# Kernel tuning notes

Measured on AMD Instinct MI355X. Metric: run time of the kernel, lower is better.

Reference implementation:

```python
import jax, jax.numpy as jnp
import numpy as np

K = 20  # kNN neighbors
HEADS = 4
DIM_HEAD = 32


def setup_inputs() -> dict:
    key = jax.random.key(0)
    ks = jax.random.split(key, 20)
    B, N = 8, 2048
    s = 0.05
    inp = {
        "x": jax.random.normal(ks[0], (B, N, 3), dtype=jnp.float32),
        "batch": jnp.zeros((B, N), dtype=jnp.int32),
        # EdgeConv1: Linear(2*3, 64) -> ReLU -> Linear(64, 64)
        "ec1_w1": jax.random.normal(ks[1], (6, 64), jnp.float32) * s,
        "ec1_b1": jnp.zeros((64,), jnp.float32),
        "ec1_w2": jax.random.normal(ks[2], (64, 64), jnp.float32) * s,
        "ec1_b2": jnp.zeros((64,), jnp.float32),
        # EdgeConv2: Linear(2*64, 64) -> ReLU -> Linear(64, 128)
        "ec2_w1": jax.random.normal(ks[3], (128, 64), jnp.float32) * s,
        "ec2_b1": jnp.zeros((64,), jnp.float32),
        "ec2_w2": jax.random.normal(ks[4], (64, 128), jnp.float32) * s,
        "ec2_b2": jnp.zeros((128,), jnp.float32),
        # SelfAttention: to_qkv Linear(128, 384, bias=False); fc_out Linear(128,128)
        "qkv_w": jax.random.normal(ks[5], (128, 384), jnp.float32) * s,
        "out_w": jax.random.normal(ks[6], (128, 128), jnp.float32) * s,
        "out_b": jnp.zeros((128,), jnp.float32),
        # refine MLP: 384 -> 128 -> 64 -> num_classes(20)
        "r1_w": jax.random.normal(ks[7], (384, 128), jnp.float32) * s,
        "r1_b": jnp.zeros((128,), jnp.float32),
        "r2_w": jax.random.normal(ks[8], (128, 64), jnp.float32) * s,
        "r2_b": jnp.zeros((64,), jnp.float32),
        "r3_w": jax.random.normal(ks[9], (64, 20), jnp.float32) * s,
        "r3_b": jnp.zeros((20,), jnp.float32),
    }
    return inp


def _edge_conv(x, w1, b1, w2, b2):
    # x: [B, N, C]. Dynamic kNN in feature space, edge feat [x_i, x_j - x_i],
    # MLP, max over neighbors.
    sq = jnp.sum(x * x, axis=-1)                       # [B, N]
    d = sq[:, :, None] + sq[:, None, :] - 2.0 * jnp.einsum("bnc,bmc->bnm", x, x)
    _, idx = jax.lax.top_k(-d, K)                      # [B, N, K]
    nbr = jax.vmap(lambda xb, ib: xb[ib])(x, idx)      # [B, N, K, C]
    xi = jnp.broadcast_to(x[:, :, None, :], nbr.shape)
    e = jnp.concatenate([xi, nbr - xi], axis=-1)       # [B, N, K, 2C]
    h = jax.nn.relu(e @ w1 + b1) @ w2 + b2             # [B, N, K, out]
    return jnp.max(h, axis=2)                          # [B, N, out]


def _attention(x, qkv_w, out_w, out_b):
    B, N, C = x.shape
    qkv = x @ qkv_w                                    # [B, N, 3C]
    q, k, v = jnp.split(qkv, 3, axis=-1)
    def heads(t):
        return t.reshape(B, N, HEADS, DIM_HEAD).transpose(0, 2, 1, 3)  # [B,H,N,Dh]
    q, k, v = heads(q), heads(k), heads(v)
    scale = DIM_HEAD ** -0.5
    attn = jax.nn.softmax(jnp.einsum("bhnd,bhmd->bhnm", q, k) * scale, axis=-1)
    out = jnp.einsum("bhnm,bhmd->bhnd", attn, v)
    out = out.transpose(0, 2, 1, 3).reshape(B, N, C)
    return out @ out_w + out_b


def reference(x, batch, ec1_w1, ec1_b1, ec1_w2, ec1_b2,
              ec2_w1, ec2_b1, ec2_w2, ec2_b2,
              qkv_w, out_w, out_b,
              r1_w, r1_b, r2_w, r2_b, r3_w, r3_b):
    local = _edge_conv(x, ec1_w1, ec1_b1, ec1_w2, ec1_b2)        # [B,N,64]
    local = _edge_conv(local, ec2_w1, ec2_b1, ec2_w2, ec2_b2)    # [B,N,128]
    glob = jnp.max(local, axis=1, keepdims=True)                 # [B,1,128]
    glob = jnp.broadcast_to(glob, local.shape)                   # [B,N,128]
    att = _attention(local, qkv_w, out_w, out_b)                 # [B,N,128]
    comb = jnp.concatenate([local, glob, att], axis=-1)          # [B,N,384]
    h = jax.nn.relu(comb @ r1_w + r1_b)
    h = jax.nn.relu(h @ r2_w + r2_b)
    logits = h @ r3_w + r3_b
    return jax.nn.log_softmax(logits, axis=-1)
```

## Files before the change

kernel.cpp:

```cpp
#include <hip/hip_runtime.h>
#include <hip/hip_bf16.h>

#define BB 8
#define NN 2048
#define KK 20
#define BBNN (BB * NN)

typedef __hip_bfloat16 bf16;
typedef unsigned short u16;
typedef __attribute__((ext_vector_type(8))) short short8;
typedef __attribute__((ext_vector_type(4))) float f32x4;

__device__ __forceinline__ float b2f(bf16 v) { return __bfloat162float(v); }

template<int C>
__global__ __launch_bounds__(256) void sqT_kernel(const float* __restrict__ xin,
                                                  float* __restrict__ sq,
                                                  float* __restrict__ xT) {
    int t = blockIdx.x * 256 + threadIdx.x;
    if (t >= BBNN) return;
    const float* p = xin + (size_t)t * C;
    float s = 0.f;
    for (int c = 0; c < C; ++c) {
        float v = p[c];
        s += v * v;
        xT[(size_t)c * BBNN + t] = v;
    }
    sq[t] = s;
}

template<int C>
__global__ __launch_bounds__(512, 4) void knn1_kernel(
        const float* __restrict__ xrows,
        const float* __restrict__ xT,
        const float* __restrict__ sq,
        u16* __restrict__ idx_out) {
    __shared__ __align__(16) float xs[C][2048];
    const int blk = blockIdx.x;
    const int b = blk >> 8;
    const int tile = blk & 255;
    const int w = threadIdx.x >> 6;
    const int s = threadIdx.x & 63;
    const int tid = threadIdx.x;
    const int iA = tile * 8 + w;
    const int bn0 = b * NN;

    float dA[32];
    #pragma unroll
    for (int r = 0; r < 32; ++r) dA[r] = 0.f;

    for (int u = tid; u < C * 512; u += 512) {
        int row = u / 512, c4 = u % 512;
        *(float4*)&xs[row][c4 * 4] =
            *(const float4*)(xT + (size_t)row * BBNN + bn0 + c4 * 4);
    }
    __syncthreads();

    const int qbase = __builtin_amdgcn_readfirstlane((bn0 + iA) * C);
    float xq[C];
    #pragma unroll
    for (int cc = 0; cc < C; ++cc) xq[cc] = xrows[qbase + cc];

    #pragma unroll
    for (int t = 0; t < 8; ++t) {
        float a0 = 0.f, a1 = 0.f, a2 = 0.f, a3 = 0.f;
        #pragma unroll
        for (int cc = 0; cc < C; ++cc) {
            float4 xv = *(const float4*)&xs[cc][t * 256 + s * 4];
            float q = xq[cc];
            a0 += q * xv.x; a1 += q * xv.y; a2 += q * xv.z; a3 += q * xv.w;
        }
        dA[t * 4 + 0] += a0; dA[t * 4 + 1] += a1;
        dA[t * 4 + 2] += a2; dA[t * 4 + 3] += a3;
    }
    const float sqi = sq[bn0 + iA];
    #pragma unroll
    for (int r = 0; r < 32; ++r) {
        int j = ((r >> 2) << 8) + (s << 2) + (r & 3);
        dA[r] = (sqi + sq[bn0 + j]) - 2.f * dA[r];
    }

    unsigned rm = 0u;
    float m1 = INFINITY, m2 = INFINITY;
    int j1 = 0x7fffffff, j2 = 0x7fffffff;
    #pragma unroll
    for (int r = 0; r < 32; ++r) {
        int j = ((r >> 2) << 8) + (s << 2) + (r & 3);
        float d = dA[r];
        bool l1 = d < m1, l2 = d < m2;
        m2 = l1 ? m1 : (l2 ? d : m2);
        j2 = l1 ? j1 : (l2 ? j : j2);
        m1 = l1 ? d : m1;  j1 = l1 ? j : j1;
    }
    for (int k = 0; k < KK; ++k) {
        if (__any(j1 < 0)) {
            if (j1 < 0) {
                m1 = INFINITY; m2 = INFINITY; j1 = 0x7fffffff; j2 = 0x7fffffff;
                #pragma unroll
                for (int r = 0; r < 32; ++r) {
                    int j = ((r >> 2) << 8) + (s << 2) + (r & 3);
                    float d = (rm & (1u << r)) ? INFINITY : dA[r];
                    bool l1 = d < m1, l2 = d < m2;
                    m2 = l1 ? m1 : (l2 ? d : m2);
                    j2 = l1 ? j1 : (l2 ? j : j2);
                    m1 = l1 ? d : m1;  j1 = l1 ? j : j1;
                }
            }
        }
        float rd = m1; int rj = j1;
        #pragma unroll
        for (int m = 1; m < 64; m <<= 1) {
            float od = __shfl_xor(rd, m); int oj = __shfl_xor(rj, m);
            if (od < rd || (od == rd && oj < rj)) { rd = od; rj = oj; }
        }
        if (s == 0) idx_out[(size_t)(bn0 + iA) * KK + k] = (u16)rj;
        if (k + 1 < KK) {
            if (s == ((rj >> 2) & 63)) {
                int rr = ((rj >> 8) << 2) + (rj & 3);
                rm |= (1u << rr);
                m1 = m2; j1 = j2; m2 = INFINITY; j2 = -1;
            }
        }
    }
}

template<int C, int CH>
__global__ __launch_bounds__(512, 4) void knn_fast_kernel(
        const float* __restrict__ xrows,
        const float* __restrict__ xT,
        const float* __restrict__ sq,
        u16* __restrict__ idx_out) {
    __shared__ __align__(16) float xs[CH][2048];
    const int blk = blockIdx.x;
    const int b = blk >> 7;
    const int tile = blk & 127;
    const int w = threadIdx.x >> 6;
    const int s = threadIdx.x & 63;
    const int iA = tile * 16 + w * 2;
    const int bn0 = b * NN;
    constexpr int NCH = C / CH;

    float dA[32], dB[32];
    #pragma unroll
    for (int r = 0; r < 32; ++r) { dA[r] = 0.f; dB[r] = 0.f; }

    const int qbase = __builtin_amdgcn_readfirstlane((bn0 + iA) * C);

    for (int ch = 0; ch < NCH; ++ch) {
        __syncthreads();
        for (int u = threadIdx.x; u < CH * 512; u += 512) {
            int row = u >> 9, c4 = u & 511;
            *(float4*)&xs[row][c4 * 4] =
                *(const float4*)(xT + (size_t)(ch * CH + row) * BBNN + bn0 + c4 * 4);
        }
        __syncthreads();
        float xqA[CH], xqB[CH];
        #pragma unroll
        for (int cc = 0; cc < CH; ++cc) {
            xqA[cc] = xrows[qbase + ch * CH + cc];
            xqB[cc] = xrows[qbase + C + ch * CH + cc];
        }
        #pragma unroll
        for (int t = 0; t < 8; ++t) {
            float aA0 = 0.f, aA1 = 0.f, aA2 = 0.f, aA3 = 0.f;
            float aB0 = 0.f, aB1 = 0.f, aB2 = 0.f, aB3 = 0.f;
            #pragma unroll
            for (int cc = 0; cc < CH; ++cc) {
                float4 xv = *(const float4*)&xs[cc][t * 256 + s * 4];
                float qA = xqA[cc], qB = xqB[cc];
                aA0 += qA * xv.x; aA1 += qA * xv.y; aA2 += qA * xv.z; aA3 += qA * xv.w;
                aB0 += qB * xv.x; aB1 += qB * xv.y; aB2 += qB * xv.z; aB3 += qB * xv.w;
            }
            dA[t * 4 + 0] += aA0; dA[t * 4 + 1] += aA1;
            dA[t * 4 + 2] += aA2; dA[t * 4 + 3] += aA3;
            dB[t * 4 + 0] += aB0; dB[t * 4 + 1] += aB1;
            dB[t * 4 + 2] += aB2; dB[t * 4 + 3] += aB3;
        }
    }
    const float sqiA = sq[bn0 + iA];
    const float sqiB = sq[bn0 + iA + 1];
    #pragma unroll
    for (int r = 0; r < 32; ++r) {
        int j = ((r >> 2) << 8) + (s << 2) + (r & 3);
        float sqj = sq[bn0 + j];
        dA[r] = (sqiA + sqj) - 2.f * dA[r];
        dB[r] = (sqiB + sqj) - 2.f * dB[r];
    }

    unsigned rmA = 0u, rmB = 0u;
    float m1A = INFINITY, m2A = INFINITY, m1B = INFINITY, m2B = INFINITY;
    int j1A = 0x7fffffff, j2A = 0x7fffffff, j1B = 0x7fffffff, j2B = 0x7fffffff;
    #pragma unroll
    for (int r = 0; r < 32; ++r) {
        int j = ((r >> 2) << 8) + (s << 2) + (r & 3);
        float d = dA[r];
        bool l1 = d < m1A, l2 = d < m2A;
        m2A = l1 ? m1A : (l2 ? d : m2A);
        j2A = l1 ? j1A : (l2 ? j : j2A);
        m1A = l1 ? d : m1A;  j1A = l1 ? j : j1A;
        d = dB[r];
        l1 = d < m1B; l2 = d < m2B;
        m2B = l1 ? m1B : (l2 ? d : m2B);
        j2B = l1 ? j1B : (l2 ? j : j2B);
        m1B = l1 ? d : m1B;  j1B = l1 ? j : j1B;
    }

    for (int k = 0; k < KK; ++k) {
        if (__any(j1A < 0)) {
            if (j1A < 0) {
                m1A = INFINITY; m2A = INFINITY; j1A = 0x7fffffff; j2A = 0x7fffffff;
                #pragma unroll
                for (int r = 0; r < 32; ++r) {
                    int j = ((r >> 2) << 8) + (s << 2) + (r & 3);
                    float d = (rmA & (1u << r)) ? INFINITY : dA[r];
                    bool l1 = d < m1A, l2 = d < m2A;
                    m2A = l1 ? m1A : (l2 ? d : m2A);
                    j2A = l1 ? j1A : (l2 ? j : j2A);
                    m1A = l1 ? d : m1A;  j1A = l1 ? j : j1A;
                }
            }
        }
        if (__any(j1B < 0)) {
            if (j1B < 0) {
                m1B = INFINITY; m2B = INFINITY; j1B = 0x7fffffff; j2B = 0x7fffffff;
                #pragma unroll
                for (int r = 0; r < 32; ++r) {
                    int j = ((r >> 2) << 8) + (s << 2) + (r & 3);
                    float d = (rmB & (1u << r)) ? INFINITY : dB[r];
                    bool l1 = d < m1B, l2 = d < m2B;
                    m2B = l1 ? m1B : (l2 ? d : m2B);
                    j2B = l1 ? j1B : (l2 ? j : j2B);
                    m1B = l1 ? d : m1B;  j1B = l1 ? j : j1B;
                }
            }
        }
        float rdA = m1A, rdB = m1B; int rjA = j1A, rjB = j1B;
        #pragma unroll
        for (int m = 1; m < 64; m <<= 1) {
            float odA = __shfl_xor(rdA, m); int ojA = __shfl_xor(rjA, m);
            float odB = __shfl_xor(rdB, m); int ojB = __shfl_xor(rjB, m);
            if (odA < rdA || (odA == rdA && ojA < rjA)) { rdA = odA; rjA = ojA; }
            if (odB < rdB || (odB == rdB && ojB < rjB)) { rdB = odB; rjB = ojB; }
        }
        if (s == 0) {
            idx_out[(size_t)(bn0 + iA) * KK + k]     = (u16)rjA;
            idx_out[(size_t)(bn0 + iA + 1) * KK + k] = (u16)rjB;
        }
        if (k + 1 < KK) {
            if (s == ((rjA >> 2) & 63)) {
                int rr = ((rjA >> 8) << 2) + (rjA & 3);
                rmA |= (1u << rr);
                m1A = m2A; j1A = j2A; m2A = INFINITY; j2A = -1;
            }
            if (s == ((rjB >> 2) & 63)) {
                int rr = ((rjB >> 8) << 2) + (rjB & 3);
                rmB |= (1u << rr);
                m1B = m2B; j1B = j2B; m2B = INFINITY; j2B = -1;
            }
        }
    }
}

template<int CIN>
__global__ __launch_bounds__(256) void gemmG_kernel(const float* __restrict__ xin,
                                                    const float* __restrict__ w1,
                                                    float* __restrict__ G) {
    __shared__ __align__(16) float xr[16][CIN];
    const int bn0 = blockIdx.x * 16;
    const int tid = threadIdx.x;
    for (int p = tid; p < 16 * CIN; p += 256)
        xr[p / CIN][p % CIN] = xin[(size_t)bn0 * CIN + p];
    const int h = tid & 63, rgrp = tid >> 6;
    float wcol[CIN];
    #pragma unroll
    for (int c = 0; c < CIN; ++c) wcol[c] = w1[(CIN + c) * 64 + h];
    __syncthreads();
    #pragma unroll
    for (int rq = 0; rq < 4; ++rq) {
        const int rr = rgrp + rq * 4;
        float a = 0.f;
        if constexpr (CIN % 4 == 0) {
            #pragma unroll
            for (int c4 = 0; c4 < CIN / 4; ++c4) {
                float4 hv = *(const float4*)&xr[rr][c4 * 4];
                a += hv.x * wcol[c4 * 4 + 0];
                a += hv.y * wcol[c4 * 4 + 1];
                a += hv.z * wcol[c4 * 4 + 2];
                a += hv.w * wcol[c4 * 4 + 3];
            }
        } else {
            #pragma unroll
            for (int c = 0; c < CIN; ++c) a += xr[rr][c] * wcol[c];
        }
        G[(size_t)(bn0 + rr) * 64 + h] = a;
    }
}

template<int CIN, int COUT, bool BF16OUT>
__global__ __launch_bounds__(256) void edgeconv3_kernel(
        const float* __restrict__ xin, const u16* __restrict__ knn,
        const float* __restrict__ w1, const float* __restrict__ b1,
        const float* __restrict__ w2, const float* __restrict__ b2,
        const float* __restrict__ G, void* __restrict__ out) {
    constexpr int NS = 4;
    constexpr int KPS = KK / NS;
    const int bn0 = blockIdx.x * 4;
    const int b = bn0 >> 11;
    const int tid = threadIdx.x;
    __shared__ __align__(16) float xr[4][CIN];
    __shared__ __align__(16) float h1s[4][KK][64];
    __shared__ float pms[4][NS][COUT];
    __shared__ int js[4][KK];

    for (int p = tid; p < 4 * CIN; p += 256)
        xr[p / CIN][p % CIN] = xin[(size_t)bn0 * CIN + p];
    if (tid < 4 * KK) {
        int j = knn[(size_t)(bn0 + tid / KK) * KK + (tid % KK)];
        js[tid / KK][tid % KK] = (j < NN) ? j : 0;
    }
    __syncthreads();

    {
        const int pp = tid >> 6, h = tid & 63;
        float w1col[CIN];
        #pragma unroll
        for (int c = 0; c < CIN; ++c) w1col[c] = w1[c * 64 + h];
        float u = b1[h];
        if constexpr (CIN % 4 == 0) {
            #pragma unroll
            for (int c4 = 0; c4 < CIN / 4; ++c4) {
                float4 hv = *(const float4*)&xr[pp][c4 * 4];
                u += hv.x * w1col[c4 * 4 + 0];
                u += hv.y * w1col[c4 * 4 + 1];
                u += hv.z * w1col[c4 * 4 + 2];
                u += hv.w * w1col[c4 * 4 + 3];
            }
        } else {
            #pragma unroll
            for (int c = 0; c < CIN; ++c) u += xr[pp][c] * w1col[c];
        }
        u -= G[(size_t)(bn0 + pp) * 64 + h];
        const float* Gb = G + (size_t)b * NN * 64 + h;
        for (int k = 0; k < KK; ++k) {
            float gj = Gb[(size_t)js[pp][k] * 64];
            h1s[pp][k][h] = fmaxf(u + gj, 0.f);
        }
    }
    __syncthreads();

    if constexpr (COUT == 128) {
        const int o = tid & 63, ks = tid >> 6;
        float wcolA[64], wcolB[64];
        #pragma unroll
        for (int c = 0; c < 64; ++c) {
            wcolA[c] = w2[c * COUT + o];
            wcolB[c] = w2[c * COUT + o + 64];
        }
        #pragma unroll
        for (int pp = 0; pp < 4; ++pp) {
            float mxA = -INFINITY, mxB = -INFINITY;
            for (int k = ks * KPS; k < (ks + 1) * KPS; ++k) {
                float accA = 0.f, accB = 0.f;
                #pragma unroll
                for (int c4 = 0; c4 < 16; ++c4) {
                    float4 hv = *(const float4*)&h1s[pp][k][c4 * 4];
                    accA += hv.x * wcolA[c4 * 4 + 0];
                    accA += hv.y * wcolA[c4 * 4 + 1];
                    accA += hv.z * wcolA[c4 * 4 + 2];
                    accA += hv.w * wcolA[c4 * 4 + 3];
                    accB += hv.x * wcolB[c4 * 4 + 0];
                    accB += hv.y * wcolB[c4 * 4 + 1];
                    accB += hv.z * wcolB[c4 * 4 + 2];
                    accB += hv.w * wcolB[c4 * 4 + 3];
                }
                mxA = fmaxf(mxA, accA);
                mxB = fmaxf(mxB, accB);
            }
            pms[pp][ks][o] = mxA;
            pms[pp][ks][o + 64] = mxB;
        }
    } else {
        const int o = tid % COUT, ks = tid / COUT;
        float wcol[64];
        #pragma unroll
        for (int c = 0; c < 64; ++c) wcol[c] = w2[c * COUT + o];
        #pragma unroll
        for (int pp = 0; pp < 4; ++pp) {
            float mx = -INFINITY;
            for (int k = ks * KPS; k < (ks + 1) * KPS; ++k) {
                float acc = 0.f;
                #pragma unroll
                for (int c4 = 0; c4 < 16; ++c4) {
                    float4 hv = *(const float4*)&h1s[pp][k][c4 * 4];
                    acc += hv.x * wcol[c4 * 4 + 0];
                    acc += hv.y * wcol[c4 * 4 + 1];
                    acc += hv.z * wcol[c4 * 4 + 2];
                    acc += hv.w * wcol[c4 * 4 + 3];
                }
                mx = fmaxf(mx, acc);
            }
            pms[pp][ks][o] = mx;
        }
    }
    __syncthreads();
    for (int idx = tid; idx < 4 * COUT; idx += 256) {
        int pp = idx / COUT, oo = idx % COUT;
        float mx = pms[pp][0][oo];
        #pragma unroll
        for (int s2 = 1; s2 < NS; ++s2) mx = fmaxf(mx, pms[pp][s2][oo]);
        mx += b2[oo];
        if (BF16OUT) ((bf16*)out)[(size_t)(bn0 + pp) * COUT + oo] = __float2bfloat16(mx);
        else         ((float*)out)[(size_t)(bn0 + pp) * COUT + oo] = mx;
    }
}

__global__ __launch_bounds__(128) void gmax1_kernel(const bf16* __restrict__ f2,
                                                    float* __restrict__ pmax) {
    const int b = blockIdx.x >> 4, ch = blockIdx.x & 15, c = threadIdx.x;
    float m = -INFINITY;
    const bf16* base = f2 + ((size_t)(b * NN + ch * 128)) * 128 + c;
    for (int n = 0; n < 128; ++n) m = fmaxf(m, b2f(base[(size_t)n * 128]));
    pmax[blockIdx.x * 128 + c] = m;
}

__global__ __launch_bounds__(128) void gmax2_kernel(const float* __restrict__ pmax,
                                                    float* __restrict__ glob) {
    const int b = blockIdx.x, c = threadIdx.x;
    float m = -INFINITY;
    for (int ch = 0; ch < 16; ++ch) m = fmaxf(m, pmax[(b * 16 + ch) * 128 + c]);
    glob[b * 128 + c] = m;
}

__global__ __launch_bounds__(256) void kvt_kernel(const bf16* __restrict__ f2,
                                                  const float* __restrict__ qkv_w,
                                                  bf16* __restrict__ kk,
                                                  bf16* __restrict__ vt) {
    const int blk = blockIdx.x;
    const int h = blk >> 10;
    const int rg = blk & 1023;
    const int bn0 = rg * 16;
    const int b = bn0 >> 11, n0 = bn0 & 2047;
    const int tid = threadIdx.x;
    __shared__ __align__(16) float f2s[16][128];
    __shared__ float vbuf[16][32];

    for (int p = tid; p < 16 * 128; p += 256) {
        int rr = p >> 7, c = p & 127;
        f2s[rr][c] = b2f(f2[(size_t)(bn0 + rr) * 128 + c]);
    }
    const int col = tid & 63, rgrp = tid >> 6;
    const int kv = col >> 5, d = col & 31;
    float wcol[128];
    #pragma unroll
    for (int c = 0; c < 128; ++c)
        wcol[c] = qkv_w[c * 384 + 128 + kv * 128 + h * 32 + d];
    __syncthreads();

    #pragma unroll
    for (int rq = 0; rq < 4; ++rq) {
        const int rr = rgrp + rq * 4;
        float acc = 0.f;
        #pragma unroll
        for (int c4 = 0; c4 < 32; ++c4) {
            float4 hv = *(const float4*)&f2s[rr][c4 * 4];
            acc += hv.x * wcol[c4 * 4 + 0];
            acc += hv.y * wcol[c4 * 4 + 1];
            acc += hv.z * wcol[c4 * 4 + 2];
            acc += hv.w * wcol[c4 * 4 + 3];
        }
        if (kv == 0)
            kk[((size_t)(b * 4 + h) * 2048 + n0 + rr) * 32 + d] = __float2bfloat16(acc);
        else
            vbuf[rr][d] = acc;
    }
    __syncthreads();
    if (tid < 128) {
        int dd = tid >> 2, r2 = tid & 3;
        #pragma unroll
        for (int rq = 0; rq < 4; ++rq) {
            int r = r2 + rq * 4;
            vt[((size_t)(b * 4 + h) * 32 + dd) * 2048 + n0 + r] = __float2bfloat16(vbuf[r][dd]);
        }
    }
}

__global__ __launch_bounds__(256) void attn_mfma_kernel(
        const bf16* __restrict__ f2, const float* __restrict__ qkv_w,
        const bf16* __restrict__ kk, const bf16* __restrict__ vt,
        bf16* __restrict__ atth) {
    const int blk = blockIdx.x;
    const int tile = blk & 31;
    const int h = (blk >> 5) & 3;
    const int b = blk >> 7;
    const int tid = threadIdx.x;
    const int w = tid >> 6;
    const int lane = tid & 63;
    const int lq = lane & 15;
    const int quad = lane >> 4;
    const float scale = 0.17677669529663687f;

    __shared__ __align__(16) bf16 WqT[32][128];
    __shared__ __align__(16) bf16 pbuf[4][2][16][32];

    for (int p = tid; p < 4096; p += 256) {
        int c = p >> 5, d = p & 31;
        WqT[d][c] = __float2bfloat16(qkv_w[c * 384 + h * 32 + d]);
    }
    __syncthreads();

    const int q0 = tile * 64 + w * 16;
    const bf16* fbase = f2 + ((size_t)(b * NN + q0 + lq)) * 128;
    f32x4 qc0 = {0.f, 0.f, 0.f, 0.f}, qc1 = {0.f, 0.f, 0.f, 0.f};
    #pragma unroll
    for (int kc = 0; kc < 4; ++kc) {
        short8 af = *(const short8*)(fbase + kc * 32 + quad * 8);
        short8 b0 = *(const short8*)(&WqT[lq][kc * 32 + quad * 8]);
        short8 b1 = *(const short8*)(&WqT[16 + lq][kc * 32 + quad * 8]);
        qc0 = __builtin_amdgcn_mfma_f32_16x16x32_bf16(af, b0, qc0, 0, 0, 0);
        qc1 = __builtin_amdgcn_mfma_f32_16x16x32_bf16(af, b1, qc1, 0, 0, 0);
    }
    {
        bf16* pw = &pbuf[w][0][0][0];
        #pragma unroll
        for (int r = 0; r < 4; ++r) {
            int qq = quad * 4 + r;
            pw[qq * 32 + lq]      = __float2bfloat16(qc0[r] * scale);
            pw[qq * 32 + 16 + lq] = __float2bfloat16(qc1[r] * scale);
        }
    }
    const short8 qfrag = *(const short8*)(&pbuf[w][0][lq][quad * 8]);

    const bf16* kb = kk + (size_t)(b * 4 + h) * 2048 * 32;
    const bf16* vb = vt + (size_t)(b * 4 + h) * 32 * 2048;
    f32x4 o0 = {0.f, 0.f, 0.f, 0.f}, o1 = {0.f, 0.f, 0.f, 0.f};
    f32x4 lsum = {0.f, 0.f, 0.f, 0.f};
    const short8 ones = {(short)0x3F80, (short)0x3F80, (short)0x3F80, (short)0x3F80,
                         (short)0x3F80, (short)0x3F80, (short)0x3F80, (short)0x3F80};

    for (int ch = 0; ch < 64; ++ch) {
        const int j0 = ch * 32;
        short8 kf0 = *(const short8*)(kb + (size_t)(j0 + lq) * 32 + quad * 8);
        short8 kf1 = *(const short8*)(kb + (size_t)(j0 + 16 + lq) * 32 + quad * 8);
        f32x4 z = {0.f, 0.f, 0.f, 0.f};
        f32x4 s0 = __builtin_amdgcn_mfma_f32_16x16x32_bf16(qfrag, kf0, z, 0, 0, 0);
        f32x4 s1 = __builtin_amdgcn_mfma_f32_16x16x32_bf16(qfrag, kf1, z, 0, 0, 0);
        bf16* pw = &pbuf[w][ch & 1][0][0];
        #pragma unroll
        for (int r = 0; r < 4; ++r) {
            int qq = quad * 4 + r;
            pw[qq * 32 + lq]      = __float2bfloat16(__expf(s0[r]));
            pw[qq * 32 + 16 + lq] = __float2bfloat16(__expf(s1[r]));
        }
        short8 pf = *(const short8*)(pw + lq * 32 + quad * 8);
        short8 vf0 = *(const short8*)(vb + (size_t)lq * 2048 + j0 + quad * 8);
        short8 vf1 = *(const short8*)(vb + (size_t)(16 + lq) * 2048 + j0 + quad * 8);
        o0   = __builtin_amdgcn_mfma_f32_16x16x32_bf16(pf, vf0, o0, 0, 0, 0);
        o1   = __builtin_amdgcn_mfma_f32_16x16x32_bf16(pf, vf1, o1, 0, 0, 0);
        lsum = __builtin_amdgcn_mfma_f32_16x16x32_bf16(pf, ones, lsum, 0, 0, 0);
    }

    #pragma unroll
    for (int r = 0; r < 4; ++r) {
        int row = q0 + quad * 4 + r;
        float inv = 1.f / lsum[r];
        bf16* orow = atth + ((size_t)(b * NN + row)) * 128 + h * 32;
        orow[lq]      = __float2bfloat16(o0[r] * inv);
        orow[16 + lq] = __float2bfloat16(o1[r] * inv);
    }
}

__global__ __launch_bounds__(256) void final_kernel(
        const bf16* __restrict__ f2, const float* __restrict__ glob,
        const bf16* __restrict__ atth,
        const float* __restrict__ out_w, const float* __restrict__ out_b,
        const float* __restrict__ r1_w, const float* __restrict__ r1_b,
        const float* __restrict__ r2_w, const float* __restrict__ r2_b,
        const float* __restrict__ r3_w, const float* __restrict__ r3_b,
        float* __restrict__ out) {
    const int bn0 = blockIdx.x * 8;
    const int b = bn0 >> 11;
    const int tid = threadIdx.x;
    __shared__ float attin[8][128], comb[8][384], h1[8][128], h2[8][64];
    __shared__ float logits[8][20], lse[8];

    for (int p = tid; p < 8 * 128; p += 256) {
        int rr = p >> 7, c = p & 127;
        attin[rr][c]      = b2f(atth[(size_t)(bn0 + rr) * 128 + c]);
        comb[rr][c]       = b2f(f2[(size_t)(bn0 + rr) * 128 + c]);
        comb[rr][128 + c] = glob[b * 128 + c];
    }
    __syncthreads();
    {
        const int col = tid & 127, r0 = (tid >> 7) * 4;
        float a0 = 0.f, a1 = 0.f, a2 = 0.f, a3 = 0.f;
        for (int c = 0; c < 128; ++c) {
            float wv = out_w[c * 128 + col];
            a0 += attin[r0 + 0][c] * wv; a1 += attin[r0 + 1][c] * wv;
            a2 += attin[r0 + 2][c] * wv; a3 += attin[r0 + 3][c] * wv;
        }
        float bb = out_b[col];
        comb[r0 + 0][256 + col] = a0 + bb; comb[r0 + 1][256 + col] = a1 + bb;
        comb[r0 + 2][256 + col] = a2 + bb; comb[r0 + 3][256 + col] = a3 + bb;
    }
    __syncthreads();
    {
        const int col = tid & 127, r0 = (tid >> 7) * 4;
        float a0 = 0.f, a1 = 0.f, a2 = 0.f, a3 = 0.f;
        for (int c = 0; c < 384; ++c) {
            float wv = r1_w[c * 128 + col];
            a0 += comb[r0 + 0][c] * wv; a1 += comb[r0 + 1][c] * wv;
            a2 += comb[r0 + 2][c] * wv; a3 += comb[r0 + 3][c] * wv;
        }
        float bb = r1_b[col];
        h1[r0 + 0][col] = fmaxf(a0 + bb, 0.f); h1[r0 + 1][col] = fmaxf(a1 + bb, 0.f);
        h1[r0 + 2][col] = fmaxf(a2 + bb, 0.f); h1[r0 + 3][col] = fmaxf(a3 + bb, 0.f);
    }
    __syncthreads();
    {
        const int col = tid & 63, r0 = (tid >> 6) * 2;
        float a0 = 0.f, a1 = 0.f;
        for (int c = 0; c < 128; ++c) {
            float wv = r2_w[c * 64 + col];
            a0 += h1[r0 + 0][c] * wv; a1 += h1[r0 + 1][c] * wv;
        }
        float bb = r2_b[col];
        h2[r0 + 0][col] = fmaxf(a0 + bb, 0.f); h2[r0 + 1][col] = fmaxf(a1 + bb, 0.f);
    }
    __syncthreads();
    if (tid < 160) {
        const int cls = tid % 20, rr = tid / 20;
        float a0 = 0.f;
        for (int c = 0; c < 64; ++c) a0 += h2[rr][c] * r3_w[c * 20 + cls];
        logits[rr][cls] = a0 + r3_b[cls];
    }
    __syncthreads();
    if (tid < 8) {
        float m = -INFINITY;
        for (int u = 0; u < 20; ++u) m = fmaxf(m, logits[tid][u]);
        float s = 0.f;
        for (int u = 0; u < 20; ++u) s += expf(logits[tid][u] - m);
        lse[tid] = m + logf(s);
    }
    __syncthreads();
    if (tid < 160) {
        int rr = tid / 20, cls = tid % 20;
        out[(size_t)(bn0 + rr) * 20 + cls] = logits[rr][cls] - lse[rr];
    }
}

extern "C" void kernel_launch(void* const* d_in, const int* in_sizes, int n_in,
                              void* d_out, int out_size, void* d_ws, size_t ws_size,
                              hipStream_t stream) {
    const float* x      = (const float*)d_in[0];
    const float* ec1_w1 = (const float*)d_in[2];
    const float* ec1_b1 = (const float*)d_in[3];
    const float* ec1_w2 = (const float*)d_in[4];
    const float* ec1_b2 = (const float*)d_in[5];
    const float* ec2_w1 = (const float*)d_in[6];
    const float* ec2_b1 = (const float*)d_in[7];
    const float* ec2_w2 = (const float*)d_in[8];
    const float* ec2_b2 = (const float*)d_in[9];
    const float* qkv_w  = (const float*)d_in[10];
    const float* out_w  = (const float*)d_in[11];
    const float* out_b  = (const float*)d_in[12];
    const float* r1_w   = (const float*)d_in[13];
    const float* r1_b   = (const float*)d_in[14];
    const float* r2_w   = (const float*)d_in[15];
    const float* r2_b   = (const float*)d_in[16];
    const float* r3_w   = (const float*)d_in[17];
    const float* r3_b   = (const float*)d_in[18];
    float* out = (float*)d_out;

    const size_t MB = 1024 * 1024;
    const size_t NEED_A = 16 * MB + 65536 + 4096;
    if (ws_size < NEED_A) return;

    char* base = (char*)d_ws;
    bf16*  f2   = (bf16*)(base);
    float* f1T  = (float*)(base);
    float* sqb  = (float*)(base + 4 * MB);
    float* f1   = (float*)(base + 4 * MB + 65536);
    u16*   knn  = (u16*)(base + 8 * MB + 65536);
    float* xT3  = (float*)(base + 8 * MB + 65536 + 655360);
    float* G    = (float*)(base + 12 * MB);
    bf16*  kkA  = (bf16*)(base + 4 * MB);
    bf16*  vtA  = (bf16*)(base + 8 * MB);
    bf16*  atth = (bf16*)(base + 12 * MB);
    float* pmax = (float*)(base + 16 * MB);
    float* glob = (float*)(base + 16 * MB + 65536);

    sqT_kernel<3><<<BBNN / 256, 256, 0, stream>>>(x, sqb, xT3);
    knn1_kernel<3><<<BB * 256, 512, 0, stream>>>(x, xT3, sqb, knn);
    gemmG_kernel<3><<<BBNN / 16, 256, 0, stream>>>(x, ec1_w1, G);
    edgeconv3_kernel<3, 64, false><<<BBNN / 4, 256, 0, stream>>>(
        x, knn, ec1_w1, ec1_b1, ec1_w2, ec1_b2, G, f1);

    sqT_kernel<64><<<BBNN / 256, 256, 0, stream>>>(f1, sqb, f1T);
    knn_fast_kernel<64, 8><<<BB * 128, 512, 0, stream>>>(f1, f1T, sqb, knn);
    gemmG_kernel<64><<<BBNN / 16, 256, 0, stream>>>(f1, ec2_w1, G);
    edgeconv3_kernel<64, 128, true><<<BBNN / 4, 256, 0, stream>>>(
        f1, knn, ec2_w1, ec2_b1, ec2_w2, ec2_b2, G, f2);

    gmax1_kernel<<<BB * 16, 128, 0, stream>>>(f2, pmax);
    gmax2_kernel<<<BB, 128, 0, stream>>>(pmax, glob);

    kvt_kernel<<<4 * BBNN / 16, 256, 0, stream>>>(f2, qkv_w, kkA, vtA);
    attn_mfma_kernel<<<BB * 4 * 32, 256, 0, stream>>>(f2, qkv_w, kkA, vtA, atth);

    final_kernel<<<BBNN / 8, 256, 0, stream>>>(
        f2, glob, atth, out_w, out_b, r1_w, r1_b, r2_w, r2_b, r3_w, r3_b, out);
}
```

Measured before the change: 686.9 us.

## Split kNN candidate range across wave halves and merge partial top-k lists

```diff
diff --git a/kernel.cpp b/kernel.cpp
--- a/kernel.cpp
+++ b/kernel.cpp
@@ -125,24 +125,29 @@
 }
 
 template<int C, int CH>
-__global__ __launch_bounds__(512, 4) void knn_fast_kernel(
+__global__ __launch_bounds__(512, 4) void knn_half_kernel(
         const float* __restrict__ xrows,
         const float* __restrict__ xT,
         const float* __restrict__ sq,
         u16* __restrict__ idx_out) {
     __shared__ __align__(16) float xs[CH][2048];
+    __shared__ float cd[8][2][KK];
+    __shared__ int   cj[8][2][KK];
     const int blk = blockIdx.x;
-    const int b = blk >> 7;
-    const int tile = blk & 127;
+    const int b = blk >> 8;
+    const int tile = blk & 255;
     const int w = threadIdx.x >> 6;
     const int s = threadIdx.x & 63;
-    const int iA = tile * 16 + w * 2;
+    const int qp = w & 3;
+    const int hf = w >> 2;
+    const int iA = tile * 8 + qp * 2;
     const int bn0 = b * NN;
+    const int base = hf * 1024;
     constexpr int NCH = C / CH;
 
-    float dA[32], dB[32];
-    #pragma unroll
-    for (int r = 0; r < 32; ++r) { dA[r] = 0.f; dB[r] = 0.f; }
+    float dA[16], dB[16];
+    #pragma unroll
+    for (int r = 0; r < 16; ++r) { dA[r] = 0.f; dB[r] = 0.f; }
 
     const int qbase = __builtin_amdgcn_readfirstlane((bn0 + iA) * C);
 
@@ -161,12 +166,12 @@
             xqB[cc] = xrows[qbase + C + ch * CH + cc];
         }
         #pragma unroll
-        for (int t = 0; t < 8; ++t) {
+        for (int t = 0; t < 4; ++t) {
             float aA0 = 0.f, aA1 = 0.f, aA2 = 0.f, aA3 = 0.f;
             float aB0 = 0.f, aB1 = 0.f, aB2 = 0.f, aB3 = 0.f;
             #pragma unroll
             for (int cc = 0; cc < CH; ++cc) {
-                float4 xv = *(const float4*)&xs[cc][t * 256 + s * 4];
+                float4 xv = *(const float4*)&xs[cc][base + t * 256 + s * 4];
                 float qA = xqA[cc], qB = xqB[cc];
                 aA0 += qA * xv.x; aA1 += qA * xv.y; aA2 += qA * xv.z; aA3 += qA * xv.w;
                 aB0 += qB * xv.x; aB1 += qB * xv.y; aB2 += qB * xv.z; aB3 += qB * xv.w;
@@ -180,8 +185,8 @@
     const float sqiA = sq[bn0 + iA];
     const float sqiB = sq[bn0 + iA + 1];
     #pragma unroll
-    for (int r = 0; r < 32; ++r) {
-        int j = ((r >> 2) << 8) + (s << 2) + (r & 3);
+    for (int r = 0; r < 16; ++r) {
+        int j = base + ((r >> 2) << 8) + (s << 2) + (r & 3);
         float sqj = sq[bn0 + j];
         dA[r] = (sqiA + sqj) - 2.f * dA[r];
         dB[r] = (sqiB + sqj) - 2.f * dB[r];
@@ -191,8 +196,8 @@
     float m1A = INFINITY, m2A = INFINITY, m1B = INFINITY, m2B = INFINITY;
     int j1A = 0x7fffffff, j2A = 0x7fffffff, j1B = 0x7fffffff, j2B = 0x7fffffff;
     #pragma unroll
-    for (int r = 0; r < 32; ++r) {
-        int j = ((r >> 2) << 8) + (s << 2) + (r & 3);
+    for (int r = 0; r < 16; ++r) {
+        int j = base + ((r >> 2) << 8) + (s << 2) + (r & 3);
         float d = dA[r];
         bool l1 = d < m1A, l2 = d < m2A;
         m2A = l1 ? m1A : (l2 ? d : m2A);
@@ -210,8 +215,8 @@
             if (j1A < 0) {
                 m1A = INFINITY; m2A = INFINITY; j1A = 0x7fffffff; j2A = 0x7fffffff;
                 #pragma unroll
-                for (int r = 0; r < 32; ++r) {
-                    int j = ((r >> 2) << 8) + (s << 2) + (r & 3);
+                for (int r = 0; r < 16; ++r) {
+                    int j = base + ((r >> 2) << 8) + (s << 2) + (r & 3);
                     float d = (rmA & (1u << r)) ? INFINITY : dA[r];
                     bool l1 = d < m1A, l2 = d < m2A;
                     m2A = l1 ? m1A : (l2 ? d : m2A);
@@ -224,8 +229,8 @@
             if (j1B < 0) {
                 m1B = INFINITY; m2B = INFINITY; j1B = 0x7fffffff; j2B = 0x7fffffff;
                 #pragma unroll
-                for (int r = 0; r < 32; ++r) {
-                    int j = ((r >> 2) << 8) + (s << 2) + (r & 3);
+                for (int r = 0; r < 16; ++r) {
+                    int j = base + ((r >> 2) << 8) + (s << 2) + (r & 3);
                     float d = (rmB & (1u << r)) ? INFINITY : dB[r];
                     bool l1 = d < m1B, l2 = d < m2B;
                     m2B = l1 ? m1B : (l2 ? d : m2B);
@@ -243,20 +248,35 @@
             if (odB < rdB || (odB == rdB && ojB < rjB)) { rdB = odB; rjB = ojB; }
         }
         if (s == 0) {
-            idx_out[(size_t)(bn0 + iA) * KK + k]     = (u16)rjA;
-            idx_out[(size_t)(bn0 + iA + 1) * KK + k] = (u16)rjB;
+            cd[qp * 2][hf][k]     = rdA; cj[qp * 2][hf][k]     = rjA;
+            cd[qp * 2 + 1][hf][k] = rdB; cj[qp * 2 + 1][hf][k] = rjB;
         }
         if (k + 1 < KK) {
             if (s == ((rjA >> 2) & 63)) {
-                int rr = ((rjA >> 8) << 2) + (rjA & 3);
+                int rr = (((rjA >> 8) & 3) << 2) + (rjA & 3);
                 rmA |= (1u << rr);
                 m1A = m2A; j1A = j2A; m2A = INFINITY; j2A = -1;
             }
             if (s == ((rjB >> 2) & 63)) {
-                int rr = ((rjB >> 8) << 2) + (rjB & 3);
+                int rr = (((rjB >> 8) & 3) << 2) + (rjB & 3);
                 rmB |= (1u << rr);
                 m1B = m2B; j1B = j2B; m2B = INFINITY; j2B = -1;
             }
+        }
+    }
+    __syncthreads();
+
+    if (threadIdx.x < 8) {
+        const int q = threadIdx.x;
+        int ia = 0, ib = 0;
+        for (int k = 0; k < KK; ++k) {
+            float da = (ia < KK) ? cd[q][0][ia] : INFINITY;
+            int   ja = (ia < KK) ? cj[q][0][ia] : 0x7fffffff;
+            float db = (ib < KK) ? cd[q][1][ib] : INFINITY;
+            int   jb = (ib < KK) ? cj[q][1][ib] : 0x7fffffff;
+            bool pick = (da < db) || (da == db && ja < jb);
+            idx_out[(size_t)(bn0 + tile * 8 + q) * KK + k] = (u16)(pick ? ja : jb);
+            ia += pick ? 1 : 0; ib += pick ? 0 : 1;
         }
     }
 }
@@ -696,7 +716,7 @@
         x, knn, ec1_w1, ec1_b1, ec1_w2, ec1_b2, G, f1);
 
     sqT_kernel<64><<<BBNN / 256, 256, 0, stream>>>(f1, sqb, f1T);
-    knn_fast_kernel<64, 8><<<BB * 128, 512, 0, stream>>>(f1, f1T, sqb, knn);
+    knn_half_kernel<64, 8><<<BB * 256, 512, 0, stream>>>(f1, f1T, sqb, knn);
     gemmG_kernel<64><<<BBNN / 16, 256, 0, stream>>>(f1, ec2_w1, G);
     edgeconv3_kernel<64, 128, true><<<BBNN / 4, 256, 0, stream>>>(
         f1, knn, ec2_w1, ec2_b1, ec2_w2, ec2_b2, G, f2);
```

After: 728.7 us. 6.1% more time.
